# Kernel tuning notes

Measured on AMD Instinct MI355X. Metric: run time of the kernel, lower is better.

## Reference

```python
import jax, jax.numpy as jnp
import numpy as np

S, B_BOX, C = 7, 2, 20
LAMBDA_COORD = 5.0
LAMBDA_NOOBJ = 0.5


def _iou(b1, b2):
    # b1, b2: [..., 4] in (cx, cy, w, h) format
    area1 = b1[..., 2] * b1[..., 3]
    area2 = b2[..., 2] * b2[..., 3]
    max_left = jnp.maximum(b1[..., 0] - b1[..., 2] / 2, b2[..., 0] - b2[..., 2] / 2)
    min_right = jnp.minimum(b1[..., 0] + b1[..., 2] / 2, b2[..., 0] + b2[..., 2] / 2)
    max_top = jnp.maximum(b1[..., 1] - b1[..., 3] / 2, b2[..., 1] - b2[..., 3] / 2)
    min_bottom = jnp.minimum(b1[..., 1] + b1[..., 3] / 2, b2[..., 1] + b2[..., 3] / 2)
    iw = jnp.maximum(min_right - max_left, 0.0)
    ih = jnp.maximum(min_bottom - max_top, 0.0)
    inter = iw * ih
    union = area1 + area2 - inter
    return jnp.where(inter > 0.0, inter / union, 0.0)


def setup_inputs() -> dict:
    key = jax.random.key(0)
    k1, k2, k3 = jax.random.split(key, 3)
    batch = 16384
    shape = (batch, S, S, C + 5 * B_BOX)  # [..., 30]
    pred = jax.random.uniform(k1, shape, dtype=jnp.float32)
    target = jax.random.uniform(k2, shape, dtype=jnp.float32)
    # objectness flag must be exactly 1.0 to trigger the obj branch
    obj_flag = jax.random.bernoulli(k3, 0.3, shape[:-1]).astype(jnp.float32)
    target = target.at[..., 0].set(obj_flag)
    return {"pred": pred, "target": target}


def reference(pred, target):
    batch = pred.shape[0]
    pred = pred.reshape(-1, S, S, C + 5 * B_BOX)
    target = target.reshape(-1, S, S, C + 5 * B_BOX)

    obj = (target[..., 0] == 1.0)          # [b,S,S] bool
    obj_f = obj.astype(pred.dtype)
    noobj_f = 1.0 - obj_f

    gt = target[..., 1:5]
    box1 = pred[..., 1:5]                   # predictor 1 box
    box2 = target[..., 6:10]                # NOTE: original code uses target's 2nd box
    iou1 = jax.lax.stop_gradient(_iou(box1, gt))
    iou2 = jax.lax.stop_gradient(_iou(box2, gt))
    resp1 = iou1 > iou2                     # predictor 1 responsible (strict >)
    r1 = resp1[..., None]

    # coord losses (responsible predictor)
    pxy = jnp.where(r1, pred[..., 1:3], pred[..., 6:8])
    txy = jnp.where(r1, target[..., 1:3], target[..., 6:8])
    pwh = jnp.where(r1, pred[..., 3:5], pred[..., 8:10])
    twh = jnp.where(r1, target[..., 3:5], target[..., 8:10])
    cell_xy = jnp.sum((pxy - txy) ** 2, axis=-1)
    cell_wh = jnp.sum((jnp.sqrt(pwh) - jnp.sqrt(twh)) ** 2, axis=-1)

    # obj confidence loss: responsible conf vs its iou
    conf_resp = jnp.where(resp1, pred[..., 0], pred[..., 5])
    iou_resp = jnp.where(resp1, iou1, iou2)
    cell_obj = (conf_resp - iou_resp) ** 2

    # noobj: non-responsible conf in obj cells; both confs in empty cells
    conf_other = jnp.where(resp1, pred[..., 5], pred[..., 0])
    cell_noobj_obj = conf_other ** 2
    cell_noobj_empty = pred[..., 0] ** 2 + pred[..., 5] ** 2

    cell_class = jnp.sum((pred[..., 10:] - target[..., 10:]) ** 2, axis=-1)

    loss_coord_xy = LAMBDA_COORD * jnp.sum(obj_f * cell_xy)
    loss_coord_wh = LAMBDA_COORD * jnp.sum(obj_f * cell_wh)
    loss_obj = jnp.sum(obj_f * cell_obj)
    loss_noobj = LAMBDA_NOOBJ * (jnp.sum(obj_f * cell_noobj_obj) + jnp.sum(noobj_f * cell_noobj_empty))
    loss_class = jnp.sum(obj_f * cell_class)
    loss = loss_coord_xy + loss_coord_wh + loss_obj + loss_noobj + loss_class

    bs = jnp.asarray(batch, pred.dtype)
    return ((loss_coord_xy + loss_coord_wh) / bs,
            loss_obj / bs,
            loss_noobj / bs,
            loss_class / bs,
            loss / bs)
```

## Files before the change

### kernel.cpp

```cpp
#include <hip/hip_runtime.h>

#define NCH 30
#define F2PC 15
#define CPB 256
#define THREADS 256
#define MAXRES 512

typedef float fvec2 __attribute__((ext_vector_type(2)));

__device__ __forceinline__ float iou_fn(float x1, float y1, float w1, float h1,
                                        float x2, float y2, float w2, float h2) {
    float a1 = w1 * h1, a2 = w2 * h2;
    float left  = fmaxf(x1 - w1 * 0.5f, x2 - w2 * 0.5f);
    float right = fminf(x1 + w1 * 0.5f, x2 + w2 * 0.5f);
    float top   = fmaxf(y1 - h1 * 0.5f, y2 - h2 * 0.5f);
    float bot   = fminf(y1 + h1 * 0.5f, y2 + h2 * 0.5f);
    float iw = fmaxf(right - left, 0.0f);
    float ih = fmaxf(bot - top, 0.0f);
    float inter = iw * ih;
    float uni = a1 + a2 - inter;
    return (inter > 0.0f) ? (inter / uni) : 0.0f;
}

__device__ __forceinline__ void cell_losses(const float* p, const float* t,
                                            float& coord, float& lobj,
                                            float& lnoobj, float& lclass) {
    float obj_f = (t[0] == 1.0f) ? 1.0f : 0.0f;

    float iou1 = iou_fn(p[1], p[2], p[3], p[4], t[1], t[2], t[3], t[4]);
    float iou2 = iou_fn(t[6], t[7], t[8], t[9], t[1], t[2], t[3], t[4]);
    bool r = iou1 > iou2;

    float px = r ? p[1] : p[6], py = r ? p[2] : p[7];
    float pw = r ? p[3] : p[8], ph = r ? p[4] : p[9];
    float tx = r ? t[1] : t[6], ty = r ? t[2] : t[7];
    float tw = r ? t[3] : t[8], th = r ? t[4] : t[9];

    float dx = px - tx, dy = py - ty;
    float cxy = dx * dx + dy * dy;
    float swv = sqrtf(pw) - sqrtf(tw), shv = sqrtf(ph) - sqrtf(th);
    float cwh = swv * swv + shv * shv;

    float conf_resp  = r ? p[0] : p[5];
    float iou_resp   = r ? iou1 : iou2;
    float conf_other = r ? p[5] : p[0];
    float dconf = conf_resp - iou_resp;

    coord  += obj_f * (cxy + cwh);
    lobj   += obj_f * dconf * dconf;
    lnoobj += obj_f * conf_other * conf_other
            + (1.0f - obj_f) * (p[0] * p[0] + p[5] * p[5]);

    float cls = 0.0f;
#pragma unroll
    for (int i = 10; i < NCH; i++) { float e = p[i] - t[i]; cls += e * e; }
    lclass += obj_f * cls;
}

__global__ __launch_bounds__(THREADS) void yolo_main(
        const fvec2* __restrict__ pred2, const fvec2* __restrict__ targ2,
        float4* __restrict__ partials, int nchunks_full, int n_cells) {
    __shared__ fvec2 sp[CPB * F2PC];
    __shared__ fvec2 st[CPB * F2PC];

    const int tid = threadIdx.x;
    float coord = 0.f, lobj = 0.f, lnoobj = 0.f, lclass = 0.f;

    fvec2 rp[F2PC], rt[F2PC];

    int c = blockIdx.x;
    bool have = c < nchunks_full;
    if (have) {
        const long long b = (long long)c * (CPB * F2PC);
#pragma unroll
        for (int k = 0; k < F2PC; k++) {
            rp[k] = __builtin_nontemporal_load(pred2 + b + tid + k * THREADS);
            rt[k] = __builtin_nontemporal_load(targ2 + b + tid + k * THREADS);
        }
    }

    while (have) {
        int cn = c + gridDim.x;
        bool have_n = cn < nchunks_full;

        __syncthreads();
#pragma unroll
        for (int k = 0; k < F2PC; k++) {
            sp[tid + k * THREADS] = rp[k];
            st[tid + k * THREADS] = rt[k];
        }
        __syncthreads();

        if (have_n) {
            const long long b = (long long)cn * (CPB * F2PC);
#pragma unroll
            for (int k = 0; k < F2PC; k++) {
                rp[k] = __builtin_nontemporal_load(pred2 + b + tid + k * THREADS);
                rt[k] = __builtin_nontemporal_load(targ2 + b + tid + k * THREADS);
            }
        }

        {
            float p[NCH], t[NCH];
            const fvec2* pp = sp + tid * F2PC;
            const fvec2* tp = st + tid * F2PC;
#pragma unroll
            for (int k = 0; k < F2PC; k++) { fvec2 v = pp[k]; p[2 * k] = v.x; p[2 * k + 1] = v.y; }
#pragma unroll
            for (int k = 0; k < F2PC; k++) { fvec2 v = tp[k]; t[2 * k] = v.x; t[2 * k + 1] = v.y; }
            cell_losses(p, t, coord, lobj, lnoobj, lclass);
        }

        c = cn; have = have_n;
    }

    if (blockIdx.x == 0) {
        int cell = nchunks_full * CPB + tid;
        if (cell < n_cells) {
            float p[NCH], t[NCH];
            const fvec2* pp = pred2 + (long long)cell * F2PC;
            const fvec2* tp = targ2 + (long long)cell * F2PC;
#pragma unroll
            for (int k = 0; k < F2PC; k++) { fvec2 v = pp[k]; p[2 * k] = v.x; p[2 * k + 1] = v.y; }
#pragma unroll
            for (int k = 0; k < F2PC; k++) { fvec2 v = tp[k]; t[2 * k] = v.x; t[2 * k + 1] = v.y; }
            cell_losses(p, t, coord, lobj, lnoobj, lclass);
        }
    }

#pragma unroll
    for (int off = 32; off > 0; off >>= 1) {
        coord  += __shfl_down(coord, off);
        lobj   += __shfl_down(lobj, off);
        lnoobj += __shfl_down(lnoobj, off);
        lclass += __shfl_down(lclass, off);
    }

    __shared__ float red[4][4];
    int lane = tid & 63;
    int wid  = tid >> 6;
    if (lane == 0) {
        red[wid][0] = coord; red[wid][1] = lobj;
        red[wid][2] = lnoobj; red[wid][3] = lclass;
    }
    __syncthreads();
    if (tid == 0) {
        float s0 = 0.f, s1 = 0.f, s2 = 0.f, s3 = 0.f;
        for (int w = 0; w < 4; w++) {
            s0 += red[w][0]; s1 += red[w][1];
            s2 += red[w][2]; s3 += red[w][3];
        }
        partials[blockIdx.x] = make_float4(s0, s1, s2, s3);
    }
}

__global__ __launch_bounds__(THREADS) void yolo_reduce(
        const float4* __restrict__ partials, int nparts,
        float* __restrict__ out, double inv_bs) {
    double s0 = 0.0, s1 = 0.0, s2 = 0.0, s3 = 0.0;
    for (int i = threadIdx.x; i < nparts; i += THREADS) {
        float4 v = partials[i];
        s0 += (double)v.x; s1 += (double)v.y;
        s2 += (double)v.z; s3 += (double)v.w;
    }
#pragma unroll
    for (int off = 32; off > 0; off >>= 1) {
        s0 += __shfl_down(s0, off);
        s1 += __shfl_down(s1, off);
        s2 += __shfl_down(s2, off);
        s3 += __shfl_down(s3, off);
    }
    __shared__ double red[4][4];
    int lane = threadIdx.x & 63;
    int wid  = threadIdx.x >> 6;
    if (lane == 0) {
        red[wid][0] = s0; red[wid][1] = s1;
        red[wid][2] = s2; red[wid][3] = s3;
    }
    __syncthreads();
    if (threadIdx.x == 0) {
        double a0 = 0, a1 = 0, a2 = 0, a3 = 0;
        for (int w = 0; w < 4; w++) {
            a0 += red[w][0]; a1 += red[w][1];
            a2 += red[w][2]; a3 += red[w][3];
        }
        double cd = a0 * 5.0 * inv_bs;
        double o  = a1 * inv_bs;
        double n  = a2 * 0.5 * inv_bs;
        double cl = a3 * inv_bs;
        out[0] = (float)cd;
        out[1] = (float)o;
        out[2] = (float)n;
        out[3] = (float)cl;
        out[4] = (float)(cd + o + n + cl);
    }
}

extern "C" void kernel_launch(void* const* d_in, const int* in_sizes, int n_in,
                              void* d_out, int out_size, void* d_ws, size_t ws_size,
                              hipStream_t stream) {
    const fvec2* pred2 = (const fvec2*)d_in[0];
    const fvec2* targ2 = (const fvec2*)d_in[1];
    float* out = (float*)d_out;
    float4* partials = (float4*)d_ws;

    int n_cells = in_sizes[0] / NCH;
    int batch   = n_cells / 49;
    int nchunks_full = n_cells / CPB;

    int grid;
    if (nchunks_full <= 0) {
        grid = 1;
    } else {
        int iters = (nchunks_full + MAXRES - 1) / MAXRES;
        grid = (nchunks_full + iters - 1) / iters;
    }

    yolo_main<<<grid, THREADS, 0, stream>>>(pred2, targ2, partials, nchunks_full, n_cells);
    yolo_reduce<<<1, THREADS, 0, stream>>>(partials, grid, out, 1.0 / (double)batch);
}
```

Baseline: 190.6 us.

## Replace LDS-staged chunk pipeline with direct per-thread float4 loads of cell pairs

Drops the shared-memory transpose, the register double-buffering and the persistent grid of at most 512 blocks. Each thread now loads two adjacent cells (240 bytes, 15 float4s) straight from global memory and processes them, and the grid is sized to cover all pairs, capped by the workspace size. This removes LDS traffic and barriers. In exchange, loads are strided per thread and no longer coalesced, and many more partials go to the reduce kernel, which may make it slower.

```diff
diff --git a/kernel.cpp b/kernel.cpp
--- a/kernel.cpp
+++ b/kernel.cpp
@@ -2,11 +2,11 @@
 
 #define NCH 30
 #define F2PC 15
-#define CPB 256
+#define F4PP 15
 #define THREADS 256
-#define MAXRES 512
 
 typedef float fvec2 __attribute__((ext_vector_type(2)));
+typedef float fvec4 __attribute__((ext_vector_type(4)));
 
 __device__ __forceinline__ float iou_fn(float x1, float y1, float w1, float h1,
                                         float x2, float y2, float w2, float h2) {
@@ -58,68 +58,35 @@
 }
 
 __global__ __launch_bounds__(THREADS) void yolo_main(
-        const fvec2* __restrict__ pred2, const fvec2* __restrict__ targ2,
-        float4* __restrict__ partials, int nchunks_full, int n_cells) {
-    __shared__ fvec2 sp[CPB * F2PC];
-    __shared__ fvec2 st[CPB * F2PC];
-
+        const fvec4* __restrict__ pred4, const fvec4* __restrict__ targ4,
+        float4* __restrict__ partials, int n_pairs, int n_cells) {
     const int tid = threadIdx.x;
     float coord = 0.f, lobj = 0.f, lnoobj = 0.f, lclass = 0.f;
 
-    fvec2 rp[F2PC], rt[F2PC];
-
-    int c = blockIdx.x;
-    bool have = c < nchunks_full;
-    if (have) {
-        const long long b = (long long)c * (CPB * F2PC);
+    for (long long i = (long long)blockIdx.x * THREADS + tid;
+         i < n_pairs;
+         i += (long long)gridDim.x * THREADS) {
+        const long long c0 = 2 * i;
+        if (c0 + 1 < (long long)n_cells) {
+            float p[2 * NCH], t[2 * NCH];
+            const fvec4* pp = pred4 + i * F4PP;
+            const fvec4* tp = targ4 + i * F4PP;
 #pragma unroll
-        for (int k = 0; k < F2PC; k++) {
-            rp[k] = __builtin_nontemporal_load(pred2 + b + tid + k * THREADS);
-            rt[k] = __builtin_nontemporal_load(targ2 + b + tid + k * THREADS);
-        }
-    }
-
-    while (have) {
-        int cn = c + gridDim.x;
-        bool have_n = cn < nchunks_full;
-
-        __syncthreads();
+            for (int k = 0; k < F4PP; k++) {
+                fvec4 v = pp[k];
+                p[4 * k] = v.x; p[4 * k + 1] = v.y; p[4 * k + 2] = v.z; p[4 * k + 3] = v.w;
+            }
 #pragma unroll
-        for (int k = 0; k < F2PC; k++) {
-            sp[tid + k * THREADS] = rp[k];
-            st[tid + k * THREADS] = rt[k];
-        }
-        __syncthreads();
-
-        if (have_n) {
-            const long long b = (long long)cn * (CPB * F2PC);
-#pragma unroll
-            for (int k = 0; k < F2PC; k++) {
-                rp[k] = __builtin_nontemporal_load(pred2 + b + tid + k * THREADS);
-                rt[k] = __builtin_nontemporal_load(targ2 + b + tid + k * THREADS);
+            for (int k = 0; k < F4PP; k++) {
+                fvec4 v = tp[k];
+                t[4 * k] = v.x; t[4 * k + 1] = v.y; t[4 * k + 2] = v.z; t[4 * k + 3] = v.w;
             }
-        }
-
-        {
+            cell_losses(p, t, coord, lobj, lnoobj, lclass);
+            cell_losses(p + NCH, t + NCH, coord, lobj, lnoobj, lclass);
+        } else if (c0 < (long long)n_cells) {
             float p[NCH], t[NCH];
-            const fvec2* pp = sp + tid * F2PC;
-            const fvec2* tp = st + tid * F2PC;
-#pragma unroll
-            for (int k = 0; k < F2PC; k++) { fvec2 v = pp[k]; p[2 * k] = v.x; p[2 * k + 1] = v.y; }
-#pragma unroll
-            for (int k = 0; k < F2PC; k++) { fvec2 v = tp[k]; t[2 * k] = v.x; t[2 * k + 1] = v.y; }
-            cell_losses(p, t, coord, lobj, lnoobj, lclass);
-        }
-
-        c = cn; have = have_n;
-    }
-
-    if (blockIdx.x == 0) {
-        int cell = nchunks_full * CPB + tid;
-        if (cell < n_cells) {
-            float p[NCH], t[NCH];
-            const fvec2* pp = pred2 + (long long)cell * F2PC;
-            const fvec2* tp = targ2 + (long long)cell * F2PC;
+            const fvec2* pp = reinterpret_cast<const fvec2*>(pred4) + c0 * F2PC;
+            const fvec2* tp = reinterpret_cast<const fvec2*>(targ4) + c0 * F2PC;
 #pragma unroll
             for (int k = 0; k < F2PC; k++) { fvec2 v = pp[k]; p[2 * k] = v.x; p[2 * k + 1] = v.y; }
 #pragma unroll
@@ -199,23 +166,21 @@
 extern "C" void kernel_launch(void* const* d_in, const int* in_sizes, int n_in,
                               void* d_out, int out_size, void* d_ws, size_t ws_size,
                               hipStream_t stream) {
-    const fvec2* pred2 = (const fvec2*)d_in[0];
-    const fvec2* targ2 = (const fvec2*)d_in[1];
+    const fvec4* pred4 = (const fvec4*)d_in[0];
+    const fvec4* targ4 = (const fvec4*)d_in[1];
     float* out = (float*)d_out;
     float4* partials = (float4*)d_ws;
 
     int n_cells = in_sizes[0] / NCH;
     int batch   = n_cells / 49;
-    int nchunks_full = n_cells / CPB;
+    int n_pairs = (n_cells + 1) / 2;
 
-    int grid;
-    if (nchunks_full <= 0) {
-        grid = 1;
-    } else {
-        int iters = (nchunks_full + MAXRES - 1) / MAXRES;
-        grid = (nchunks_full + iters - 1) / iters;
-    }
+    int grid = (n_pairs + THREADS - 1) / THREADS;
+    if (grid < 1) grid = 1;
 
-    yolo_main<<<grid, THREADS, 0, stream>>>(pred2, targ2, partials, nchunks_full, n_cells);
+    int max_parts = (int)(ws_size / sizeof(float4));
+    if (max_parts >= 1 && grid > max_parts) grid = max_parts;
+
+    yolo_main<<<grid, THREADS, 0, stream>>>(pred4, targ4, partials, n_pairs, n_cells);
     yolo_reduce<<<1, THREADS, 0, stream>>>(partials, grid, out, 1.0 / (double)batch);
 }
```

New measurement: 212.1 us. 1.11x slower.
